# Kernel optimization log

Hardware: AMD Instinct MI355X
Metric: run time of the kernel (lower is better)

## Reference

```python
import jax, jax.numpy as jnp
import numpy as np

D = 1024

def setup_inputs() -> dict:
    key = jax.random.key(0)
    ks = jax.random.split(key, 9)
    B, S = 4, 2048
    s = 1.0 / np.sqrt(D)
    return {
        "query": jax.random.normal(ks[0], (B, S, D), jnp.float32),
        "key": jax.random.normal(ks[1], (B, S, D), jnp.float32),
        "value": jax.random.normal(ks[2], (B, S, D), jnp.float32),
        "Wq": jax.random.normal(ks[3], (D, D), jnp.float32) * s,
        "bq": jax.random.normal(ks[4], (D,), jnp.float32) * 0.01,
        "Wk": jax.random.normal(ks[5], (D, D), jnp.float32) * s,
        "bk": jax.random.normal(ks[6], (D,), jnp.float32) * 0.01,
        "Wv": jax.random.normal(ks[7], (D, D), jnp.float32) * s,
        "bv": jax.random.normal(ks[8], (D,), jnp.float32) * 0.01,
    }

def reference(query, key, value, Wq, bq, Wk, bk, Wv, bv):
    scale = 1.0 / (query.shape[-1] ** 0.5)
    q = jnp.einsum('bsd,ed->bse', query, Wq) + bq  # nn.Linear: x @ W.T + b
    k = jnp.einsum('bsd,ed->bse', key, Wk) + bk
    v = jnp.einsum('bsd,ed->bse', value, Wv) + bv
    scores = jnp.einsum('bqd,bkd->bqk', q, k) * scale  # [B, Sq, Skv]
    w = jax.nn.softmax(scores, axis=-1)
    return jnp.einsum('bqk,bkd->bqd', w, v)
```

## Files before the change

### kernel.cpp

```cpp
#include <hip/hip_runtime.h>

typedef __bf16 bf16x8 __attribute__((ext_vector_type(8)));
typedef float f32x4 __attribute__((ext_vector_type(4)));
typedef unsigned short u16x8 __attribute__((ext_vector_type(8)));

__device__ inline unsigned short f2bf(float f) {
  union { float f; unsigned u; } a; a.f = f;
  return (unsigned short)((a.u + 0x7fffu + ((a.u >> 16) & 1u)) >> 16);
}
__device__ inline float bf2f(unsigned short h) {
  union { unsigned u; float f; } a; a.u = ((unsigned)h) << 16;
  return a.f;
}

struct CvtArgs {
  const float* src[6];
  unsigned short* dst[6];
};

__global__ __launch_bounds__(256) void cvt6(CvtArgs a) {
  long long i = (long long)blockIdx.x * 256 + threadIdx.x;
  int idx; long long off;
  if (i < 6291456LL) { idx = (int)(i >> 21); off = i & ((1LL << 21) - 1); }
  else { long long j = i - 6291456LL; idx = 3 + (int)(j >> 18); off = j & ((1LL << 18) - 1); }
  float4 v = ((const float4*)a.src[idx])[off];
  ushort4 o;
  o.x = f2bf(v.x); o.y = f2bf(v.y); o.z = f2bf(v.z); o.w = f2bf(v.w);
  ((ushort4*)a.dst[idx])[off] = o;
}

#define EPI_PROJ 0
#define EPI_SCALE 1

struct G256 {
  const unsigned short* A;
  const unsigned short* B;
  unsigned short* C;
  unsigned short* outQ; unsigned short* outK; unsigned short* outV;
  const float* biasQ; const float* biasK; const float* biasV;
  long long batchA, batchB, batchC;
  int lda, ldb, ldc, K;
  float scale;
};

#define G2L(gp, lp) __builtin_amdgcn_global_load_lds( \
    (const __attribute__((address_space(1))) void*)(gp), \
    (__attribute__((address_space(3))) void*)(lp), 16, 0, 0)

#define MFMA_(d, a, b) d = __builtin_amdgcn_mfma_f32_16x16x32_bf16(a, b, d, 0, 0, 0)

template<int EPI>
__global__ __launch_bounds__(512, 2) void gemm256(G256 p) {
  extern __shared__ char smem[];
  char* smA = smem;
  char* smB = smem + 65536;

  const int tid = threadIdx.x;
  const int lane = tid & 63;
  const int wave = tid >> 6;
  const int wm = wave >> 2;
  const int wn = wave & 3;

  const int gx = gridDim.x, gy = gridDim.y;
  const int nwg = gx * gy * (int)gridDim.z;
  int orig = blockIdx.x + gx * (blockIdx.y + gy * blockIdx.z);
  int q = nwg >> 3, r = nwg & 7;
  int xcd = orig & 7, sl = orig >> 3;
  int wg = (xcd < r ? xcd * (q + 1) : r * (q + 1) + (xcd - r) * q) + sl;
  int bx = wg % gx;
  int t2 = wg / gx;
  int by = t2 % gy;
  int z  = t2 / gy;

  const int m0 = by << 8, n0 = bx << 8;

  const long long lda2 = (long long)p.lda * 2;
  const long long ldb2 = (long long)p.ldb * 2;
  const char* Abase = (const char*)(p.A + (long long)z * p.batchA) + (long long)m0 * lda2;
  const char* Bbase = (const char*)(p.B + (long long)z * p.batchB) + (long long)n0 * ldb2;

  const int trow = tid >> 3;
  const int cs = (((tid & 7) ^ (trow & 7)) << 4);
  const char* srcA = Abase + (long long)trow * lda2 + cs;
  const char* srcB = Bbase + (long long)trow * ldb2 + cs;

  const int NT = p.K >> 6;

  const int arow = ((wm << 7) + (lane & 15)) << 7;
  const int brow = ((wn << 6) + (lane & 15)) << 7;
  const int csw = (lane & 7) << 4;
  const int ck0 = (((lane >> 4) << 4)) ^ csw;
  const int ck1 = ((((lane >> 4) << 4)) | 64) ^ csw;

  f32x4 acc[8][4];
#pragma unroll
  for (int i = 0; i < 8; ++i)
#pragma unroll
    for (int j = 0; j < 4; ++j) acc[i][j] = (f32x4){0.f, 0.f, 0.f, 0.f};

  bf16x8 af[4][2], bfr[4][2];

  auto issueB = [&](int t) {
    char* d = smB + ((t & 1) << 15) + (wave << 10);
    const char* s = srcB + (long long)t * 128;
#pragma unroll
    for (int c = 0; c < 4; ++c)
      G2L(s + (long long)c * (ldb2 << 6), d + (c << 13));
  };
  auto issueA = [&](int t) {
    char* d = smA + ((t & 1) << 15) + (wave << 10);
    const char* s = srcA + (long long)t * 128;
#pragma unroll
    for (int c = 0; c < 4; ++c)
      G2L(s + (long long)c * (lda2 << 6), d + (c << 13));
  };

  issueB(0); issueA(0); issueB(1); issueA(1);
  asm volatile("s_waitcnt vmcnt(8)" ::: "memory");
  __builtin_amdgcn_s_barrier();

  auto step = [&](int t, int b) {
    const char* ra = smA + (b << 15);
    const char* rb = smB + (b << 15);
#pragma unroll
    for (int mi = 0; mi < 4; ++mi) {
      af[mi][0] = *(const bf16x8*)(ra + arow + (mi << 11) + ck0);
      af[mi][1] = *(const bf16x8*)(ra + arow + (mi << 11) + ck1);
    }
#pragma unroll
    for (int ni = 0; ni < 2; ++ni) {
      bfr[ni][0] = *(const bf16x8*)(rb + brow + (ni << 11) + ck0);
      bfr[ni][1] = *(const bf16x8*)(rb + brow + (ni << 11) + ck1);
    }
    __builtin_amdgcn_s_barrier();
    asm volatile("s_waitcnt lgkmcnt(0)" ::: "memory");
    __builtin_amdgcn_sched_barrier(0);
    __builtin_amdgcn_s_setprio(1);
#pragma unroll
    for (int mi = 0; mi < 4; ++mi)
#pragma unroll
      for (int ni = 0; ni < 2; ++ni) {
        MFMA_(acc[mi][ni], af[mi][0], bfr[ni][0]);
        MFMA_(acc[mi][ni], af[mi][1], bfr[ni][1]);
      }
    __builtin_amdgcn_s_setprio(0);
    __builtin_amdgcn_s_barrier();
#pragma unroll
    for (int ni = 2; ni < 4; ++ni) {
      bfr[ni][0] = *(const bf16x8*)(rb + brow + (ni << 11) + ck0);
      bfr[ni][1] = *(const bf16x8*)(rb + brow + (ni << 11) + ck1);
    }
    __builtin_amdgcn_s_barrier();
    asm volatile("s_waitcnt lgkmcnt(0)" ::: "memory");
    __builtin_amdgcn_sched_barrier(0);
    __builtin_amdgcn_s_setprio(1);
#pragma unroll
    for (int mi = 0; mi < 4; ++mi)
#pragma unroll
      for (int ni = 2; ni < 4; ++ni) {
        MFMA_(acc[mi][ni], af[mi][0], bfr[ni][0]);
        MFMA_(acc[mi][ni], af[mi][1], bfr[ni][1]);
      }
    __builtin_amdgcn_s_setprio(0);
    __builtin_amdgcn_s_barrier();
#pragma unroll
    for (int mi = 0; mi < 4; ++mi) {
      af[mi][0] = *(const bf16x8*)(ra + arow + ((mi + 4) << 11) + ck0);
      af[mi][1] = *(const bf16x8*)(ra + arow + ((mi + 4) << 11) + ck1);
    }
    if (t + 2 < NT) issueB(t + 2);
    __builtin_amdgcn_s_barrier();
    asm volatile("s_waitcnt lgkmcnt(0)" ::: "memory");
    __builtin_amdgcn_sched_barrier(0);
    __builtin_amdgcn_s_setprio(1);
#pragma unroll
    for (int mi = 0; mi < 4; ++mi)
#pragma unroll
      for (int ni = 0; ni < 2; ++ni) {
        MFMA_(acc[mi + 4][ni], af[mi][0], bfr[ni][0]);
        MFMA_(acc[mi + 4][ni], af[mi][1], bfr[ni][1]);
      }
    __builtin_amdgcn_s_setprio(0);
    __builtin_amdgcn_s_barrier();
    if (t + 2 < NT) issueA(t + 2);
    __builtin_amdgcn_s_barrier();
    __builtin_amdgcn_s_setprio(1);
#pragma unroll
    for (int mi = 0; mi < 4; ++mi)
#pragma unroll
      for (int ni = 2; ni < 4; ++ni) {
        MFMA_(acc[mi + 4][ni], af[mi][0], bfr[ni][0]);
        MFMA_(acc[mi + 4][ni], af[mi][1], bfr[ni][1]);
      }
    __builtin_amdgcn_s_setprio(0);
    if (t + 2 < NT) { asm volatile("s_waitcnt vmcnt(8)" ::: "memory"); }
    else            { asm volatile("s_waitcnt vmcnt(0)" ::: "memory"); }
    __builtin_amdgcn_s_barrier();
  };

  for (int t = 0; t < NT; t += 2) { step(t, 0); step(t + 1, 1); }

  const int c0 = lane & 15;
  const int r0 = (lane >> 4) << 2;
  if constexpr (EPI == EPI_SCALE) {
    unsigned short* Cz = p.C + (long long)z * p.batchC;
#pragma unroll
    for (int mi = 0; mi < 8; ++mi) {
      const int grow = m0 + (wm << 7) + (mi << 4) + r0;
#pragma unroll
      for (int ni = 0; ni < 4; ++ni) {
        const int gcol = n0 + (wn << 6) + (ni << 4) + c0;
#pragma unroll
        for (int rr = 0; rr < 4; ++rr)
          Cz[(long long)(grow + rr) * p.ldc + gcol] = f2bf(acc[mi][ni][rr] * p.scale);
      }
    }
  } else {
    if (z < 2) {
      unsigned short* O = (z == 0) ? p.outQ : p.outK;
      const float* bias = (z == 0) ? p.biasQ : p.biasK;
#pragma unroll
      for (int mi = 0; mi < 8; ++mi) {
        const int grow = m0 + (wm << 7) + (mi << 4) + r0;
#pragma unroll
        for (int ni = 0; ni < 4; ++ni) {
          const int gcol = n0 + (wn << 6) + (ni << 4) + c0;
          const float bb = bias[gcol];
#pragma unroll
          for (int rr = 0; rr < 4; ++rr)
            O[(long long)(grow + rr) * 1024 + gcol] = f2bf(acc[mi][ni][rr] + bb);
        }
      }
    } else {
#pragma unroll
      for (int mi = 0; mi < 8; ++mi) {
        const int grow = m0 + (wm << 7) + (mi << 4) + r0;
        const int bb = grow >> 11, s = grow & 2047;
#pragma unroll
        for (int ni = 0; ni < 4; ++ni) {
          const int d = n0 + (wn << 6) + (ni << 4) + c0;
          const float ba = p.biasV[d];
          ushort4 pk;
          pk.x = f2bf(acc[mi][ni][0] + ba);
          pk.y = f2bf(acc[mi][ni][1] + ba);
          pk.z = f2bf(acc[mi][ni][2] + ba);
          pk.w = f2bf(acc[mi][ni][3] + ba);
          *(ushort4*)(p.outV + ((long long)bb << 21) + (long long)d * 2048 + s) = pk;
        }
      }
    }
  }
}

#define EPI_OUT 3

template<int EPI>
__global__ __launch_bounds__(256, 2) void gemm_bt(
    const unsigned short* __restrict__ A,
    const unsigned short* __restrict__ B,
    void* __restrict__ Cv,
    const float* __restrict__ bias,
    int lda, int ldb, int ldc, int K, float scale,
    long long batchA, long long batchB, long long batchC)
{
  __shared__ unsigned short sA[128 * 64];
  __shared__ unsigned short sB[128 * 64];
  const int tid = threadIdx.x;
  const int lane = tid & 63;
  const int wave = tid >> 6;
  const int wm = wave >> 1, wn = wave & 1;
  const int z = blockIdx.z;
  const int m0 = blockIdx.y * 128, n0 = blockIdx.x * 128;

  const char* Ab = (const char*)(A + (long long)z * batchA + (long long)m0 * lda);
  const char* Bb = (const char*)(B + (long long)z * batchB + (long long)n0 * ldb);
  const int lda2 = lda * 2, ldb2 = ldb * 2;

  f32x4 acc[4][4];
#pragma unroll
  for (int i = 0; i < 4; ++i)
#pragma unroll
    for (int j = 0; j < 4; ++j) acc[i][j] = (f32x4){0.f, 0.f, 0.f, 0.f};

  const int laneoff = (lane & 15) * 128 + (lane >> 4) * 16;

  const int nkt = K >> 6;
  for (int kt = 0; kt < nkt; ++kt) {
    const int kb = kt * 128;
#pragma unroll
    for (int i = 0; i < 4; ++i) {
      unsigned o = (unsigned)(i * 4096 + wave * 1024 + lane * 16);
      unsigned row = o >> 7, cb = o & 127u;
      G2L(Ab + (long long)row * lda2 + kb + cb, (char*)sA + i * 4096 + wave * 1024);
      G2L(Bb + (long long)row * ldb2 + kb + cb, (char*)sB + i * 4096 + wave * 1024);
    }
    __syncthreads();

    const char* sAc = (const char*)sA;
    const char* sBc = (const char*)sB;
#pragma unroll
    for (int kk = 0; kk < 2; ++kk) {
      bf16x8 af[4], bfr[4];
#pragma unroll
      for (int mi = 0; mi < 4; ++mi)
        af[mi] = *(const bf16x8*)(sAc + (wm * 64 + mi * 16) * 128 + kk * 64 + laneoff);
#pragma unroll
      for (int ni = 0; ni < 4; ++ni)
        bfr[ni] = *(const bf16x8*)(sBc + (wn * 64 + ni * 16) * 128 + kk * 64 + laneoff);
#pragma unroll
      for (int mi = 0; mi < 4; ++mi)
#pragma unroll
        for (int ni = 0; ni < 4; ++ni)
          acc[mi][ni] = __builtin_amdgcn_mfma_f32_16x16x32_bf16(af[mi], bfr[ni], acc[mi][ni], 0, 0, 0);
    }
    __syncthreads();
  }

  const int col16 = lane & 15;
  const int r0 = (lane >> 4) * 4;
#pragma unroll
  for (int mi = 0; mi < 4; ++mi) {
#pragma unroll
    for (int ni = 0; ni < 4; ++ni) {
      const int gcol = n0 + wn * 64 + ni * 16 + col16;
#pragma unroll
      for (int rr = 0; rr < 4; ++rr) {
        const int grow = m0 + wm * 64 + mi * 16 + r0 + rr;
        const float val = acc[mi][ni][rr] * scale;
        const size_t off = (size_t)z * batchC + (size_t)grow * ldc + gcol;
        ((float*)Cv)[off] = val;
      }
    }
  }
}

__global__ __launch_bounds__(256) void softmax_rows(unsigned short* __restrict__ S) {
  const size_t row = blockIdx.x;
  unsigned short* pp = S + row * 2048;
  const int t = threadIdx.x, lane = t & 63, wave = t >> 6;
  u16x8 h = ((const u16x8*)pp)[t];
  float x[8];
#pragma unroll
  for (int j = 0; j < 8; ++j) x[j] = bf2f(h[j]);
  float m = x[0];
#pragma unroll
  for (int j = 1; j < 8; ++j) m = fmaxf(m, x[j]);
#pragma unroll
  for (int off = 32; off >= 1; off >>= 1) m = fmaxf(m, __shfl_xor(m, off, 64));
  __shared__ float rmax[4], rsum[4];
  if (lane == 0) rmax[wave] = m;
  __syncthreads();
  m = fmaxf(fmaxf(rmax[0], rmax[1]), fmaxf(rmax[2], rmax[3]));
  float e[8], sum = 0.f;
#pragma unroll
  for (int j = 0; j < 8; ++j) { e[j] = __expf(x[j] - m); sum += e[j]; }
#pragma unroll
  for (int off = 32; off >= 1; off >>= 1) sum += __shfl_xor(sum, off, 64);
  if (lane == 0) rsum[wave] = sum;
  __syncthreads();
  sum = rsum[0] + rsum[1] + rsum[2] + rsum[3];
  const float inv = 1.f / sum;
  u16x8 o;
#pragma unroll
  for (int j = 0; j < 8; ++j) o[j] = f2bf(e[j] * inv);
  ((u16x8*)pp)[t] = o;
}

extern "C" void kernel_launch(void* const* d_in, const int* in_sizes, int n_in,
                              void* d_out, int out_size, void* d_ws, size_t ws_size,
                              hipStream_t stream) {
  const float* q  = (const float*)d_in[0];
  const float* k  = (const float*)d_in[1];
  const float* v  = (const float*)d_in[2];
  const float* Wq = (const float*)d_in[3];
  const float* bq = (const float*)d_in[4];
  const float* Wk = (const float*)d_in[5];
  const float* bk = (const float*)d_in[6];
  const float* Wv = (const float*)d_in[7];
  const float* bv = (const float*)d_in[8];

  unsigned short* Xb = (unsigned short*)d_ws;
  unsigned short* Wb = Xb + 25165824;
  unsigned short* qb = Wb + 3145728;
  unsigned short* kb = qb + 8388608;
  unsigned short* vT = kb + 8388608;
  unsigned short* S  = Xb;

  (void)hipFuncSetAttribute((const void*)gemm256<EPI_PROJ>,
      hipFuncAttributeMaxDynamicSharedMemorySize, 131072);
  (void)hipFuncSetAttribute((const void*)gemm256<EPI_SCALE>,
      hipFuncAttributeMaxDynamicSharedMemorySize, 131072);

  CvtArgs ca;
  ca.src[0] = q;  ca.src[1] = k;  ca.src[2] = v;
  ca.src[3] = Wq; ca.src[4] = Wk; ca.src[5] = Wv;
  ca.dst[0] = Xb;            ca.dst[1] = Xb + 8388608; ca.dst[2] = Xb + 16777216;
  ca.dst[3] = Wb;            ca.dst[4] = Wb + 1048576; ca.dst[5] = Wb + 2097152;
  cvt6<<<27648, 256, 0, stream>>>(ca);

  G256 gp{};
  gp.A = Xb;  gp.batchA = 8388608; gp.lda = 1024;
  gp.B = Wb;  gp.batchB = 1048576; gp.ldb = 1024;
  gp.outQ = qb; gp.outK = kb; gp.outV = vT;
  gp.biasQ = bq; gp.biasK = bk; gp.biasV = bv;
  gp.K = 1024; gp.scale = 1.f;
  gemm256<EPI_PROJ><<<dim3(4, 32, 3), 512, 131072, stream>>>(gp);

  G256 gs{};
  gs.A = qb; gs.batchA = 2097152; gs.lda = 1024;
  gs.B = kb; gs.batchB = 2097152; gs.ldb = 1024;
  gs.C = S;  gs.batchC = 4194304; gs.ldc = 2048;
  gs.K = 1024; gs.scale = 0.03125f;
  gemm256<EPI_SCALE><<<dim3(8, 8, 4), 512, 131072, stream>>>(gs);

  softmax_rows<<<8192, 256, 0, stream>>>(S);

  gemm_bt<EPI_OUT><<<dim3(8, 16, 4), 256, 0, stream>>>(
      S, vT, (float*)d_out, nullptr, 2048, 2048, 1024, 2048, 1.f,
      4194304LL, 2097152LL, 2097152LL);
}
```

Measured before the change: 199.4 us.

## Re-pipeline 256-tile GEMM main loop and use it for the PV GEMM

```diff
diff --git a/kernel.cpp b/kernel.cpp
--- a/kernel.cpp
+++ b/kernel.cpp
@@ -31,6 +31,7 @@
 
 #define EPI_PROJ 0
 #define EPI_SCALE 1
+#define EPI_OUT 2
 
 struct G256 {
   const unsigned short* A;
@@ -48,6 +49,7 @@
     (__attribute__((address_space(3))) void*)(lp), 16, 0, 0)
 
 #define MFMA_(d, a, b) d = __builtin_amdgcn_mfma_f32_16x16x32_bf16(a, b, d, 0, 0, 0)
+#define SB0() __builtin_amdgcn_sched_barrier(0)
 
 template<int EPI>
 __global__ __launch_bounds__(512, 2) void gemm256(G256 p) {
@@ -64,9 +66,9 @@
   const int gx = gridDim.x, gy = gridDim.y;
   const int nwg = gx * gy * (int)gridDim.z;
   int orig = blockIdx.x + gx * (blockIdx.y + gy * blockIdx.z);
-  int q = nwg >> 3, r = nwg & 7;
+  int qq = nwg >> 3, rr_ = nwg & 7;
   int xcd = orig & 7, sl = orig >> 3;
-  int wg = (xcd < r ? xcd * (q + 1) : r * (q + 1) + (xcd - r) * q) + sl;
+  int wg = (xcd < rr_ ? xcd * (qq + 1) : rr_ * (qq + 1) + (xcd - rr_) * qq) + sl;
   int bx = wg % gx;
   int t2 = wg / gx;
   int by = t2 % gy;
@@ -98,30 +100,36 @@
 #pragma unroll
     for (int j = 0; j < 4; ++j) acc[i][j] = (f32x4){0.f, 0.f, 0.f, 0.f};
 
-  bf16x8 af[4][2], bfr[4][2];
-
-  auto issueB = [&](int t) {
-    char* d = smB + ((t & 1) << 15) + (wave << 10);
+  bf16x8 af[4][2], ag[4][2], bf[2][2], bg[2][2];
+
+  auto stA03 = [&](int t) {
+    char* d = smA + ((t & 1) << 15) + (tid << 4);
+    const char* s = srcA + (long long)t * 128;
+    G2L(s, d);
+    G2L(s + (lda2 << 7), d + 16384);
+  };
+  auto stA47 = [&](int t) {
+    char* d = smA + ((t & 1) << 15) + (tid << 4);
+    const char* s = srcA + (long long)t * 128;
+    G2L(s + (lda2 << 6), d + 8192);
+    G2L(s + 3 * (lda2 << 6), d + 24576);
+  };
+  auto stB1 = [&](int t) {
+    char* d = smB + ((t & 1) << 15) + (tid << 4);
     const char* s = srcB + (long long)t * 128;
-#pragma unroll
-    for (int c = 0; c < 4; ++c)
-      G2L(s + (long long)c * (ldb2 << 6), d + (c << 13));
-  };
-  auto issueA = [&](int t) {
-    char* d = smA + ((t & 1) << 15) + (wave << 10);
-    const char* s = srcA + (long long)t * 128;
-#pragma unroll
-    for (int c = 0; c < 4; ++c)
-      G2L(s + (long long)c * (lda2 << 6), d + (c << 13));
-  };
-
-  issueB(0); issueA(0); issueB(1); issueA(1);
-  asm volatile("s_waitcnt vmcnt(8)" ::: "memory");
-  __builtin_amdgcn_s_barrier();
-
-  auto step = [&](int t, int b) {
-    const char* ra = smA + (b << 15);
-    const char* rb = smB + (b << 15);
+    G2L(s, d);
+    G2L(s + (ldb2 << 6), d + 8192);
+  };
+  auto stB2 = [&](int t) {
+    char* d = smB + ((t & 1) << 15) + (tid << 4);
+    const char* s = srcB + (long long)t * 128;
+    G2L(s + 2 * (ldb2 << 6), d + 16384);
+    G2L(s + 3 * (ldb2 << 6), d + 24576);
+  };
+
+  auto readR0 = [&](int t) {
+    const char* ra = smA + ((t & 1) << 15);
+    const char* rb = smB + ((t & 1) << 15);
 #pragma unroll
     for (int mi = 0; mi < 4; ++mi) {
       af[mi][0] = *(const bf16x8*)(ra + arow + (mi << 11) + ck0);
@@ -129,76 +137,99 @@
     }
 #pragma unroll
     for (int ni = 0; ni < 2; ++ni) {
-      bfr[ni][0] = *(const bf16x8*)(rb + brow + (ni << 11) + ck0);
-      bfr[ni][1] = *(const bf16x8*)(rb + brow + (ni << 11) + ck1);
-    }
+      bf[ni][0] = *(const bf16x8*)(rb + brow + (ni << 11) + ck0);
+      bf[ni][1] = *(const bf16x8*)(rb + brow + (ni << 11) + ck1);
+    }
+  };
+
+  stA03(0); stA47(0); stB1(0); stB2(0);
+  stA03(1); stA47(1); stB1(1);
+  asm volatile("s_waitcnt vmcnt(6)" ::: "memory");
+  __builtin_amdgcn_s_barrier();
+  SB0();
+  readR0(0);
+
+  for (int t = 0; t < NT; ++t) {
+    const char* ra = smA + ((t & 1) << 15);
+    const char* rb = smB + ((t & 1) << 15);
+    const bool pf1 = (t + 1) < NT;
+    const bool pf2 = (t + 2) < NT;
+
+#pragma unroll
+    for (int mi = 0; mi < 4; ++mi) {
+      ag[mi][0] = *(const bf16x8*)(ra + arow + ((mi + 4) << 11) + ck0);
+      ag[mi][1] = *(const bf16x8*)(ra + arow + ((mi + 4) << 11) + ck1);
+    }
+    if (pf1) stB2(t + 1);
+    SB0();
+    __builtin_amdgcn_s_barrier();
+    asm volatile("s_waitcnt lgkmcnt(8)" ::: "memory");
+    SB0();
+    __builtin_amdgcn_s_setprio(1);
+#pragma unroll
+    for (int mi = 0; mi < 4; ++mi)
+#pragma unroll
+      for (int ni = 0; ni < 2; ++ni) {
+        MFMA_(acc[mi][ni], af[mi][0], bf[ni][0]);
+        MFMA_(acc[mi][ni], af[mi][1], bf[ni][1]);
+      }
+    __builtin_amdgcn_s_setprio(0);
+    __builtin_amdgcn_s_barrier();
+
+#pragma unroll
+    for (int ni = 0; ni < 2; ++ni) {
+      bg[ni][0] = *(const bf16x8*)(rb + brow + ((ni + 2) << 11) + ck0);
+      bg[ni][1] = *(const bf16x8*)(rb + brow + ((ni + 2) << 11) + ck1);
+    }
+    if (pf2) stA03(t + 2);
+    SB0();
+    __builtin_amdgcn_s_barrier();
+    asm volatile("s_waitcnt lgkmcnt(4)" ::: "memory");
+    SB0();
+    __builtin_amdgcn_s_setprio(1);
+#pragma unroll
+    for (int mi = 0; mi < 4; ++mi)
+#pragma unroll
+      for (int ni = 0; ni < 2; ++ni) {
+        MFMA_(acc[mi + 4][ni], ag[mi][0], bf[ni][0]);
+        MFMA_(acc[mi + 4][ni], ag[mi][1], bf[ni][1]);
+      }
+    __builtin_amdgcn_s_setprio(0);
+    __builtin_amdgcn_s_barrier();
+
+    if (pf2) stA47(t + 2);
+    SB0();
     __builtin_amdgcn_s_barrier();
     asm volatile("s_waitcnt lgkmcnt(0)" ::: "memory");
-    __builtin_amdgcn_sched_barrier(0);
+    SB0();
     __builtin_amdgcn_s_setprio(1);
 #pragma unroll
     for (int mi = 0; mi < 4; ++mi)
 #pragma unroll
       for (int ni = 0; ni < 2; ++ni) {
-        MFMA_(acc[mi][ni], af[mi][0], bfr[ni][0]);
-        MFMA_(acc[mi][ni], af[mi][1], bfr[ni][1]);
+        MFMA_(acc[mi][ni + 2], af[mi][0], bg[ni][0]);
+        MFMA_(acc[mi][ni + 2], af[mi][1], bg[ni][1]);
       }
     __builtin_amdgcn_s_setprio(0);
-    __builtin_amdgcn_s_barrier();
-#pragma unroll
-    for (int ni = 2; ni < 4; ++ni) {
-      bfr[ni][0] = *(const bf16x8*)(rb + brow + (ni << 11) + ck0);
-      bfr[ni][1] = *(const bf16x8*)(rb + brow + (ni << 11) + ck1);
-    }
-    __builtin_amdgcn_s_barrier();
-    asm volatile("s_waitcnt lgkmcnt(0)" ::: "memory");
-    __builtin_amdgcn_sched_barrier(0);
+    if (pf1) { asm volatile("s_waitcnt vmcnt(4)" ::: "memory"); }
+    __builtin_amdgcn_s_barrier();
+
+    if (pf1) readR0(t + 1);
+    if (pf2) stB1(t + 2);
+    SB0();
+    __builtin_amdgcn_s_barrier();
+    SB0();
     __builtin_amdgcn_s_setprio(1);
 #pragma unroll
     for (int mi = 0; mi < 4; ++mi)
 #pragma unroll
-      for (int ni = 2; ni < 4; ++ni) {
-        MFMA_(acc[mi][ni], af[mi][0], bfr[ni][0]);
-        MFMA_(acc[mi][ni], af[mi][1], bfr[ni][1]);
+      for (int ni = 0; ni < 2; ++ni) {
+        MFMA_(acc[mi + 4][ni + 2], ag[mi][0], bg[ni][0]);
+        MFMA_(acc[mi + 4][ni + 2], ag[mi][1], bg[ni][1]);
       }
     __builtin_amdgcn_s_setprio(0);
     __builtin_amdgcn_s_barrier();
-#pragma unroll
-    for (int mi = 0; mi < 4; ++mi) {
-      af[mi][0] = *(const bf16x8*)(ra + arow + ((mi + 4) << 11) + ck0);
-      af[mi][1] = *(const bf16x8*)(ra + arow + ((mi + 4) << 11) + ck1);
-    }
-    if (t + 2 < NT) issueB(t + 2);
-    __builtin_amdgcn_s_barrier();
-    asm volatile("s_waitcnt lgkmcnt(0)" ::: "memory");
-    __builtin_amdgcn_sched_barrier(0);
-    __builtin_amdgcn_s_setprio(1);
-#pragma unroll
-    for (int mi = 0; mi < 4; ++mi)
-#pragma unroll
-      for (int ni = 0; ni < 2; ++ni) {
-        MFMA_(acc[mi + 4][ni], af[mi][0], bfr[ni][0]);
-        MFMA_(acc[mi + 4][ni], af[mi][1], bfr[ni][1]);
-      }
-    __builtin_amdgcn_s_setprio(0);
-    __builtin_amdgcn_s_barrier();
-    if (t + 2 < NT) issueA(t + 2);
-    __builtin_amdgcn_s_barrier();
-    __builtin_amdgcn_s_setprio(1);
-#pragma unroll
-    for (int mi = 0; mi < 4; ++mi)
-#pragma unroll
-      for (int ni = 2; ni < 4; ++ni) {
-        MFMA_(acc[mi + 4][ni], af[mi][0], bfr[ni][0]);
-        MFMA_(acc[mi + 4][ni], af[mi][1], bfr[ni][1]);
-      }
-    __builtin_amdgcn_s_setprio(0);
-    if (t + 2 < NT) { asm volatile("s_waitcnt vmcnt(8)" ::: "memory"); }
-    else            { asm volatile("s_waitcnt vmcnt(0)" ::: "memory"); }
-    __builtin_amdgcn_s_barrier();
-  };
-
-  for (int t = 0; t < NT; t += 2) { step(t, 0); step(t + 1, 1); }
+  }
 
   const int c0 = lane & 15;
   const int r0 = (lane >> 4) << 2;
@@ -213,6 +244,19 @@
 #pragma unroll
         for (int rr = 0; rr < 4; ++rr)
           Cz[(long long)(grow + rr) * p.ldc + gcol] = f2bf(acc[mi][ni][rr] * p.scale);
+      }
+    }
+  } else if constexpr (EPI == EPI_OUT) {
+    float* Cz = (float*)p.C + (long long)z * p.batchC;
+#pragma unroll
+    for (int mi = 0; mi < 8; ++mi) {
+      const int grow = m0 + (wm << 7) + (mi << 4) + r0;
+#pragma unroll
+      for (int ni = 0; ni < 4; ++ni) {
+        const int gcol = n0 + (wn << 6) + (ni << 4) + c0;
+#pragma unroll
+        for (int rr = 0; rr < 4; ++rr)
+          Cz[(long long)(grow + rr) * p.ldc + gcol] = acc[mi][ni][rr] * p.scale;
       }
     }
   } else {
@@ -247,88 +291,6 @@
           pk.w = f2bf(acc[mi][ni][3] + ba);
           *(ushort4*)(p.outV + ((long long)bb << 21) + (long long)d * 2048 + s) = pk;
         }
-      }
-    }
-  }
-}
-
-#define EPI_OUT 3
-
-template<int EPI>
-__global__ __launch_bounds__(256, 2) void gemm_bt(
-    const unsigned short* __restrict__ A,
-    const unsigned short* __restrict__ B,
-    void* __restrict__ Cv,
-    const float* __restrict__ bias,
-    int lda, int ldb, int ldc, int K, float scale,
-    long long batchA, long long batchB, long long batchC)
-{
-  __shared__ unsigned short sA[128 * 64];
-  __shared__ unsigned short sB[128 * 64];
-  const int tid = threadIdx.x;
-  const int lane = tid & 63;
-  const int wave = tid >> 6;
-  const int wm = wave >> 1, wn = wave & 1;
-  const int z = blockIdx.z;
-  const int m0 = blockIdx.y * 128, n0 = blockIdx.x * 128;
-
-  const char* Ab = (const char*)(A + (long long)z * batchA + (long long)m0 * lda);
-  const char* Bb = (const char*)(B + (long long)z * batchB + (long long)n0 * ldb);
-  const int lda2 = lda * 2, ldb2 = ldb * 2;
-
-  f32x4 acc[4][4];
-#pragma unroll
-  for (int i = 0; i < 4; ++i)
-#pragma unroll
-    for (int j = 0; j < 4; ++j) acc[i][j] = (f32x4){0.f, 0.f, 0.f, 0.f};
-
-  const int laneoff = (lane & 15) * 128 + (lane >> 4) * 16;
-
-  const int nkt = K >> 6;
-  for (int kt = 0; kt < nkt; ++kt) {
-    const int kb = kt * 128;
-#pragma unroll
-    for (int i = 0; i < 4; ++i) {
-      unsigned o = (unsigned)(i * 4096 + wave * 1024 + lane * 16);
-      unsigned row = o >> 7, cb = o & 127u;
-      G2L(Ab + (long long)row * lda2 + kb + cb, (char*)sA + i * 4096 + wave * 1024);
-      G2L(Bb + (long long)row * ldb2 + kb + cb, (char*)sB + i * 4096 + wave * 1024);
-    }
-    __syncthreads();
-
-    const char* sAc = (const char*)sA;
-    const char* sBc = (const char*)sB;
-#pragma unroll
-    for (int kk = 0; kk < 2; ++kk) {
-      bf16x8 af[4], bfr[4];
-#pragma unroll
-      for (int mi = 0; mi < 4; ++mi)
-        af[mi] = *(const bf16x8*)(sAc + (wm * 64 + mi * 16) * 128 + kk * 64 + laneoff);
-#pragma unroll
-      for (int ni = 0; ni < 4; ++ni)
-        bfr[ni] = *(const bf16x8*)(sBc + (wn * 64 + ni * 16) * 128 + kk * 64 + laneoff);
-#pragma unroll
-      for (int mi = 0; mi < 4; ++mi)
-#pragma unroll
-        for (int ni = 0; ni < 4; ++ni)
-          acc[mi][ni] = __builtin_amdgcn_mfma_f32_16x16x32_bf16(af[mi], bfr[ni], acc[mi][ni], 0, 0, 0);
-    }
-    __syncthreads();
-  }
-
-  const int col16 = lane & 15;
-  const int r0 = (lane >> 4) * 4;
-#pragma unroll
-  for (int mi = 0; mi < 4; ++mi) {
-#pragma unroll
-    for (int ni = 0; ni < 4; ++ni) {
-      const int gcol = n0 + wn * 64 + ni * 16 + col16;
-#pragma unroll
-      for (int rr = 0; rr < 4; ++rr) {
-        const int grow = m0 + wm * 64 + mi * 16 + r0 + rr;
-        const float val = acc[mi][ni][rr] * scale;
-        const size_t off = (size_t)z * batchC + (size_t)grow * ldc + gcol;
-        ((float*)Cv)[off] = val;
       }
     }
   }
@@ -390,6 +352,8 @@
       hipFuncAttributeMaxDynamicSharedMemorySize, 131072);
   (void)hipFuncSetAttribute((const void*)gemm256<EPI_SCALE>,
       hipFuncAttributeMaxDynamicSharedMemorySize, 131072);
+  (void)hipFuncSetAttribute((const void*)gemm256<EPI_OUT>,
+      hipFuncAttributeMaxDynamicSharedMemorySize, 131072);
 
   CvtArgs ca;
   ca.src[0] = q;  ca.src[1] = k;  ca.src[2] = v;
@@ -415,7 +379,10 @@
 
   softmax_rows<<<8192, 256, 0, stream>>>(S);
 
-  gemm_bt<EPI_OUT><<<dim3(8, 16, 4), 256, 0, stream>>>(
-      S, vT, (float*)d_out, nullptr, 2048, 2048, 1024, 2048, 1.f,
-      4194304LL, 2097152LL, 2097152LL);
-}
+  G256 gv{};
+  gv.A = S;  gv.batchA = 4194304; gv.lda = 2048;
+  gv.B = vT; gv.batchB = 2097152; gv.ldb = 2048;
+  gv.C = (unsigned short*)d_out; gv.batchC = 2097152; gv.ldc = 1024;
+  gv.K = 2048; gv.scale = 1.f;
+  gemm256<EPI_OUT><<<dim3(4, 8, 4), 512, 131072, stream>>>(gv);
+}
```

After: 209.1 us. 1.05x slower.
